# Kernel tuning notes

Hardware: AMD Instinct MI355X
Metric: run time of the kernel (lower is better)

## Reference

```python
import jax, jax.numpy as jnp
import numpy as np

# model dims (see init_kwargs)
HID = 2048
H = 16
Q_LORA = 768
KV_LORA = 512
QK_NOPE = 128
QK_ROPE = 64
QK_HEAD = QK_NOPE + QK_ROPE  # 192
V_DIM = 128
HI = 8        # indexer heads
DI = 128      # indexer head dim
TOPK = 512    # index_topk
EPS = 1e-5
B, S = 1, 2048


def rms_norm(x, w):
    return x * jax.lax.rsqrt(jnp.mean(x * x, -1, keepdims=True) + EPS) * w


def layer_norm(x, w, b):
    m = jnp.mean(x, -1, keepdims=True)
    v = jnp.mean((x - m) ** 2, -1, keepdims=True)
    return (x - m) * jax.lax.rsqrt(v + EPS) * w + b


def rotate_half(x):
    x1, x2 = jnp.split(x, 2, axis=-1)
    return jnp.concatenate([-x2, x1], axis=-1)


def rope_bshd(x, cos, sin):
    # x: [B,S,H,D], cos/sin: [B,S,D] -> broadcast over heads (unsqueeze_dim=2)
    return x * cos[:, :, None, :] + rotate_half(x) * sin[:, :, None, :]


def setup_inputs() -> dict:
    key = jax.random.key(0)
    ks = jax.random.split(key, 16)
    std = 0.02
    hidden_states = jax.random.normal(ks[0], (B, S, HID), jnp.float32)
    # real RoPE tables, theta=10000, head_dim=QK_ROPE
    inv_freq = 1.0 / (10000.0 ** (np.arange(0, QK_ROPE, 2, dtype=np.float32) / QK_ROPE))
    freqs = np.arange(S, dtype=np.float32)[:, None] * inv_freq[None, :]  # [S, ROPE/2]
    emb = np.concatenate([freqs, freqs], axis=-1)
    cos = jnp.asarray(np.cos(emb))[None]  # [1,S,ROPE]
    sin = jnp.asarray(np.sin(emb))[None]
    w = lambda k, shp: jax.random.normal(k, shp, jnp.float32) * std
    return {
        'hidden_states': hidden_states, 'cos': cos, 'sin': sin,
        'wq_a': w(ks[1], (Q_LORA, HID)),
        'q_a_norm_w': jnp.ones((Q_LORA,), jnp.float32),
        'wq_b': w(ks[2], (H * QK_HEAD, Q_LORA)),
        'wkv_a': w(ks[3], (KV_LORA + QK_ROPE, HID)),
        'kv_a_norm_w': jnp.ones((KV_LORA,), jnp.float32),
        'wkv_b': w(ks[4], (H * (QK_NOPE + V_DIM), KV_LORA)),
        'wo': w(ks[5], (HID, H * V_DIM)),
        'idx_wq_b': w(ks[6], (HI * DI, Q_LORA)),
        'idx_wk': w(ks[7], (DI, HID)),
        'idx_k_norm_w': jnp.ones((DI,), jnp.float32),
        'idx_k_norm_b': jnp.zeros((DI,), jnp.float32),
        'idx_weights_w': w(ks[8], (HI, HID)),
    }


def reference(hidden_states, cos, sin, wq_a, q_a_norm_w, wq_b, wkv_a, kv_a_norm_w,
              wkv_b, wo, idx_wq_b, idx_wk, idx_k_norm_w, idx_k_norm_b, idx_weights_w):
    b, s, _ = hidden_states.shape
    # ---- MLA projections ----
    q_lora = rms_norm(hidden_states @ wq_a.T, q_a_norm_w)              # [B,S,Q_LORA]
    q = (q_lora @ wq_b.T).reshape(b, s, H, QK_HEAD)
    q_nope, q_rope = jnp.split(q, [QK_NOPE], axis=-1)
    q_rope = rope_bshd(q_rope, cos, sin)

    kv = hidden_states @ wkv_a.T                                        # [B,S,KV_LORA+ROPE]
    kv_lat, k_rope = jnp.split(kv, [KV_LORA], axis=-1)
    k_rope = k_rope * cos + rotate_half(k_rope) * sin                   # shared MQA rope key [B,S,ROPE]
    kv_lat = rms_norm(kv_lat, kv_a_norm_w)
    kvb = (kv_lat @ wkv_b.T).reshape(b, s, H, QK_NOPE + V_DIM)
    k_nope, value = jnp.split(kvb, [QK_NOPE], axis=-1)

    queries = jnp.concatenate([q_nope, q_rope], axis=-1)                # [B,S,H,QK_HEAD]
    keys = jnp.concatenate(
        [k_nope, jnp.broadcast_to(k_rope[:, :, None, :], (b, s, H, QK_ROPE))], axis=-1)

    # ---- lightning indexer (DSA): per-query top-k KV selection ----
    iq = (q_lora @ idx_wq_b.T).reshape(b, s, HI, DI)
    iq_rot, iq_pass = jnp.split(iq, [QK_ROPE], axis=-1)
    iq = jnp.concatenate([rope_bshd(iq_rot, cos, sin), iq_pass], axis=-1)
    ik = layer_norm(hidden_states @ idx_wk.T, idx_k_norm_w, idx_k_norm_b)  # [B,S,DI]
    ik_rot, ik_pass = jnp.split(ik, [QK_ROPE], axis=-1)
    ik = jnp.concatenate([ik_rot * cos + rotate_half(ik_rot) * sin, ik_pass], axis=-1)

    iscores = jnp.einsum('bqhd,bkd->bqhk', iq, ik) * (DI ** -0.5)       # [B,S,HI,S]
    iw = (hidden_states @ idx_weights_w.T) * (HI ** -0.5)               # [B,S,HI]
    iscore = jnp.einsum('bqh,bqhk->bqk', iw, iscores)                   # [B,S,S]

    causal = jnp.tril(jnp.ones((s, s), bool))
    iscore = jnp.where(causal[None], iscore, -1e9)
    _, topk_idx = jax.lax.top_k(iscore, TOPK)                           # [B,S,TOPK]
    allow = jnp.zeros((b, s, s), bool).at[
        jnp.arange(b)[:, None, None], jnp.arange(s)[None, :, None], topk_idx].set(True)
    allow = allow & causal[None]                                        # topk AND causal

    # ---- masked attention ----
    scale = QK_HEAD ** -0.5
    scores = jnp.einsum('bqhd,bkhd->bhqk', queries, keys) * scale       # [B,H,S,S]
    scores = jnp.where(allow[:, None], scores, -jnp.inf)
    probs = jax.nn.softmax(scores, axis=-1)
    out = jnp.einsum('bhqk,bkhd->bqhd', probs, value).reshape(b, s, H * V_DIM)
    return out @ wo.T
```

## Files before the change

kernel.cpp:

```cpp
#include <hip/hip_runtime.h>
#include <hip/hip_bf16.h>
#include <stdint.h>
#include <math.h>

#define S_LEN 2048
#define HIDDEN 2048
#define NHEAD 16
#define QLORA 768
#define KVLORA 512
#define QKNOPE 128
#define QKROPE 64
#define QKHEAD 192
#define VDIM 128
#define HIN 8
#define DIN 128
#define TOPKN 512
#define EPSF 1e-5f
#define DLAT 576
#define SCALE_ATT 0.07216878364870322f

typedef __bf16 bf16x8 __attribute__((ext_vector_type(8)));
typedef float  f32x4  __attribute__((ext_vector_type(4)));

static __device__ __forceinline__ float wave_reduce_sum(float v) {
    #pragma unroll
    for (int off = 32; off > 0; off >>= 1) v += __shfl_down(v, off);
    return v;
}

static __device__ __forceinline__ void splitw(__bf16* __restrict__ H,
                                              __bf16* __restrict__ L,
                                              size_t idx, float v) {
    __bf16 h = (__bf16)v;
    H[idx] = h;
    L[idx] = (__bf16)(v - (float)h);
}

#define PREP_BLOCKS 17280
__global__ __launch_bounds__(256) void prep_all(
        const float* __restrict__ hid,     __bf16* hidH,  __bf16* hidL,
        const float* __restrict__ wq_a,    __bf16* wqaH,  __bf16* wqaL,
        const float* __restrict__ idx_wq_b,__bf16* iwqH,  __bf16* iwqL,
        const float* __restrict__ idx_wk,  __bf16* iwkH,  __bf16* iwkL,
        const float* __restrict__ wq_b,    __bf16* wq_b_bf,
        const float* __restrict__ wkv_a,   __bf16* wkv_a_bf,
        const float* __restrict__ wkv_b,   __bf16* wkv_b_bf,
        const float* __restrict__ wo,      __bf16* wo_bf,
        __bf16* wknt) {
    int b = blockIdx.x, tid = threadIdx.x;
    const float* src; __bf16 *dH = nullptr, *dL = nullptr, *dC = nullptr;
    int base;
    if (b < 4096)        { src = hid;      dH = hidH; dL = hidL; base = b; }
    else if (b < 5632)   { src = wq_a;     dH = wqaH; dL = wqaL; base = b - 4096; }
    else if (b < 6400)   { src = idx_wq_b; dH = iwqH; dL = iwqL; base = b - 5632; }
    else if (b < 6656)   { src = idx_wk;   dH = iwkH; dL = iwkL; base = b - 6400; }
    else if (b < 8960)   { src = wq_b;     dC = wq_b_bf;  base = b - 6656; }
    else if (b < 10112)  { src = wkv_a;    dC = wkv_a_bf; base = b - 8960; }
    else if (b < 12160)  { src = wkv_b;    dC = wkv_b_bf; base = b - 10112; }
    else if (b < 16256)  { src = wo;       dC = wo_bf;    base = b - 12160; }
    else {
        int e = ((b - 16256) * 256 + tid) * 4;
        int c = e & 511, d = (e >> 9) & 127, h = e >> 16;
        f32x4 v = *(const f32x4*)(wkv_b + ((size_t)(h * 256 + d)) * 512 + c);
        #pragma unroll
        for (int j = 0; j < 4; ++j)
            wknt[(size_t)h * 65536 + (c + j) * 128 + d] = (__bf16)v[j];
        return;
    }
    int i = (base * 256 + tid) * 4;
    f32x4 v = *(const f32x4*)(src + i);
    if (dC) {
        #pragma unroll
        for (int j = 0; j < 4; ++j) dC[i + j] = (__bf16)v[j];
    } else {
        #pragma unroll
        for (int j = 0; j < 4; ++j) splitw(dH, dL, i + j, v[j]);
    }
}

#define GBM 128
#define GBN 64
#define GBK 32
template <typename OutT>
__global__ __launch_bounds__(256) void gemm_s(const __bf16* __restrict__ A,
                                              const __bf16* __restrict__ B,
                                              OutT* __restrict__ C,
                                              int M, int N, int K,
                                              int lda, int ldb, int ldc,
                                              long sA, long sB, long sC) {
    A += (size_t)blockIdx.z * sA;
    B += (size_t)blockIdx.z * sB;
    C += (size_t)blockIdx.z * sC;
    __shared__ __bf16 sAs[GBM * GBK];
    __shared__ __bf16 sBs[GBN * GBK];
    int tid = threadIdx.x;
    int lane = tid & 63, wid = tid >> 6;
    int quad = lane >> 4, l16 = lane & 15;
    int wm = wid >> 1, wn = wid & 1;
    int row0 = blockIdx.y * GBM, col0 = blockIdx.x * GBN;

    f32x4 acc[4][2] = {};
    int am = tid >> 1, ah = tid & 1;
    int bn = tid >> 2, bq = tid & 3;

    for (int k0 = 0; k0 < K; k0 += GBK) {
        const uint4* ga = (const uint4*)(A + (size_t)(row0 + am) * lda + k0 + ah * 16);
        uint4* da = (uint4*)&sAs[am * GBK + ah * 16];
        da[0] = ga[0];
        da[1] = ga[1];
        *(uint4*)&sBs[bn * GBK + bq * 8] =
            *(const uint4*)(B + (size_t)(col0 + bn) * ldb + k0 + bq * 8);
        __syncthreads();
        bf16x8 af[4], bfr[2];
        #pragma unroll
        for (int mi = 0; mi < 4; ++mi)
            af[mi] = *(const bf16x8*)&sAs[(wm * 64 + mi * 16 + l16) * GBK + quad * 8];
        #pragma unroll
        for (int ni = 0; ni < 2; ++ni)
            bfr[ni] = *(const bf16x8*)&sBs[(wn * 32 + ni * 16 + l16) * GBK + quad * 8];
        #pragma unroll
        for (int mi = 0; mi < 4; ++mi)
            #pragma unroll
            for (int ni = 0; ni < 2; ++ni)
                acc[mi][ni] = __builtin_amdgcn_mfma_f32_16x16x32_bf16(
                    af[mi], bfr[ni], acc[mi][ni], 0, 0, 0);
        __syncthreads();
    }
    #pragma unroll
    for (int mi = 0; mi < 4; ++mi)
        #pragma unroll
        for (int ni = 0; ni < 2; ++ni)
            #pragma unroll
            for (int r = 0; r < 4; ++r) {
                int row = row0 + wm * 64 + mi * 16 + quad * 4 + r;
                int col = col0 + wn * 32 + ni * 16 + l16;
                C[(size_t)row * ldc + col] = (OutT)acc[mi][ni][r];
            }
}

template <bool CAUSAL>
__global__ __launch_bounds__(256) void gemm3(const __bf16* __restrict__ Ah,
                                             const __bf16* __restrict__ Al,
                                             const __bf16* __restrict__ Bh,
                                             const __bf16* __restrict__ Bl,
                                             float* __restrict__ C,
                                             int M, int N, int K,
                                             int lda, int ldb, int ldc,
                                             int row_base) {
    int row0 = blockIdx.y * GBM + row_base, col0 = blockIdx.x * GBN;
    if (CAUSAL && col0 > row0 + GBM - 1) return;
    __shared__ __bf16 sAh[GBM * GBK], sAl[GBM * GBK];
    __shared__ __bf16 sBh[GBN * GBK], sBl[GBN * GBK];
    int tid = threadIdx.x;
    int lane = tid & 63, wid = tid >> 6;
    int quad = lane >> 4, l16 = lane & 15;
    int wm = wid >> 1, wn = wid & 1;

    f32x4 acc[4][2] = {};
    int am = tid >> 1, ah = tid & 1;
    int bn = tid >> 2, bq = tid & 3;

    for (int k0 = 0; k0 < K; k0 += GBK) {
        size_t aoff = (size_t)(row0 + am) * lda + k0 + ah * 16;
        uint4* dah = (uint4*)&sAh[am * GBK + ah * 16];
        uint4* dal = (uint4*)&sAl[am * GBK + ah * 16];
        dah[0] = ((const uint4*)(Ah + aoff))[0];
        dah[1] = ((const uint4*)(Ah + aoff))[1];
        dal[0] = ((const uint4*)(Al + aoff))[0];
        dal[1] = ((const uint4*)(Al + aoff))[1];
        size_t boff = (size_t)(col0 + bn) * ldb + k0 + bq * 8;
        *(uint4*)&sBh[bn * GBK + bq * 8] = *(const uint4*)(Bh + boff);
        *(uint4*)&sBl[bn * GBK + bq * 8] = *(const uint4*)(Bl + boff);
        __syncthreads();
        bf16x8 afh[4], afl[4], bfh[2], bfl[2];
        #pragma unroll
        for (int mi = 0; mi < 4; ++mi) {
            int o = (wm * 64 + mi * 16 + l16) * GBK + quad * 8;
            afh[mi] = *(const bf16x8*)&sAh[o];
            afl[mi] = *(const bf16x8*)&sAl[o];
        }
        #pragma unroll
        for (int ni = 0; ni < 2; ++ni) {
            int o = (wn * 32 + ni * 16 + l16) * GBK + quad * 8;
            bfh[ni] = *(const bf16x8*)&sBh[o];
            bfl[ni] = *(const bf16x8*)&sBl[o];
        }
        #pragma unroll
        for (int mi = 0; mi < 4; ++mi)
            #pragma unroll
            for (int ni = 0; ni < 2; ++ni) {
                acc[mi][ni] = __builtin_amdgcn_mfma_f32_16x16x32_bf16(
                    afl[mi], bfh[ni], acc[mi][ni], 0, 0, 0);
                acc[mi][ni] = __builtin_amdgcn_mfma_f32_16x16x32_bf16(
                    afh[mi], bfl[ni], acc[mi][ni], 0, 0, 0);
                acc[mi][ni] = __builtin_amdgcn_mfma_f32_16x16x32_bf16(
                    afh[mi], bfh[ni], acc[mi][ni], 0, 0, 0);
            }
        __syncthreads();
    }
    #pragma unroll
    for (int mi = 0; mi < 4; ++mi)
        #pragma unroll
        for (int ni = 0; ni < 2; ++ni)
            #pragma unroll
            for (int r = 0; r < 4; ++r) {
                int row = row0 + wm * 64 + mi * 16 + quad * 4 + r;
                int col = col0 + wn * 32 + ni * 16 + l16;
                C[(size_t)row * ldc + col] = acc[mi][ni][r];
            }
}

__global__ __launch_bounds__(256) void rmsnorm_split(const float* __restrict__ x,
                                                     const float* __restrict__ w,
                                                     __bf16* __restrict__ yH,
                                                     __bf16* __restrict__ yL, int ncols) {
    int row = blockIdx.x, tid = threadIdx.x;
    const float* xr = x + (size_t)row * ncols;
    float ss = 0.f;
    for (int c = tid; c < ncols; c += 256) { float v = xr[c]; ss += v * v; }
    __shared__ float red[4];
    ss = wave_reduce_sum(ss);
    if ((tid & 63) == 0) red[tid >> 6] = ss;
    __syncthreads();
    float tot = red[0] + red[1] + red[2] + red[3];
    float inv = rsqrtf(tot / (float)ncols + EPSF);
    for (int c = tid; c < ncols; c += 256)
        splitw(yH, yL, (size_t)row * ncols + c, xr[c] * inv * w[c]);
}

__global__ __launch_bounds__(256) void rope_qeff(const __bf16* __restrict__ qbuf,
                                                 const float* __restrict__ cosT,
                                                 const float* __restrict__ sinT,
                                                 __bf16* __restrict__ qeff) {
    int s = blockIdx.x;
    for (int i = threadIdx.x; i < NHEAD * 32; i += 256) {
        int h = i >> 5, d = i & 31;
        const __bf16* base = qbuf + (size_t)s * (NHEAD * QKHEAD) + h * QKHEAD + QKNOPE;
        float x1 = (float)base[d], x2 = (float)base[d + 32];
        float c1 = cosT[s * 64 + d],      s1 = sinT[s * 64 + d];
        float c2 = cosT[s * 64 + d + 32], s2 = sinT[s * 64 + d + 32];
        __bf16* o = qeff + (size_t)s * (NHEAD * DLAT) + h * DLAT + 512;
        o[d]      = (__bf16)(x1 * c1 - x2 * s1);
        o[d + 32] = (__bf16)(x2 * c2 + x1 * s2);
    }
}

__global__ __launch_bounds__(256) void kv_post(const float* __restrict__ kv,
                                               const float* __restrict__ kvw,
                                               const float* __restrict__ cosT,
                                               const float* __restrict__ sinT,
                                               __bf16* __restrict__ klat) {
    int s = blockIdx.x, tid = threadIdx.x;
    const float* row = kv + (size_t)s * DLAT;
    float ss = 0.f;
    for (int c = tid; c < KVLORA; c += 256) { float v = row[c]; ss += v * v; }
    __shared__ float red[4];
    ss = wave_reduce_sum(ss);
    if ((tid & 63) == 0) red[tid >> 6] = ss;
    __syncthreads();
    float tot = red[0] + red[1] + red[2] + red[3];
    float inv = rsqrtf(tot / (float)KVLORA + EPSF);
    __bf16* orow = klat + (size_t)s * DLAT;
    for (int c = tid; c < KVLORA; c += 256)
        orow[c] = (__bf16)(row[c] * inv * kvw[c]);
    if (tid < 32) {
        int d = tid;
        float x1 = row[KVLORA + d], x2 = row[KVLORA + d + 32];
        float c1 = cosT[s * 64 + d],      s1 = sinT[s * 64 + d];
        float c2 = cosT[s * 64 + d + 32], s2 = sinT[s * 64 + d + 32];
        orow[512 + d]      = (__bf16)(x1 * c1 - x2 * s1);
        orow[512 + d + 32] = (__bf16)(x2 * c2 + x1 * s2);
    }
}

__global__ __launch_bounds__(128) void ik_post_split(const float* __restrict__ ikraw,
                                                     const float* __restrict__ w,
                                                     const float* __restrict__ b,
                                                     const float* __restrict__ cosT,
                                                     const float* __restrict__ sinT,
                                                     __bf16* __restrict__ ikH,
                                                     __bf16* __restrict__ ikL) {
    int s = blockIdx.x, tid = threadIdx.x;
    float x = ikraw[(size_t)s * DIN + tid];
    __shared__ float redA[2], redB[2], sy[DIN];
    float sm = wave_reduce_sum(x);
    if ((tid & 63) == 0) redA[tid >> 6] = sm;
    __syncthreads();
    float mean = (redA[0] + redA[1]) / (float)DIN;
    float dx = x - mean;
    float vs = wave_reduce_sum(dx * dx);
    if ((tid & 63) == 0) redB[tid >> 6] = vs;
    __syncthreads();
    float var = (redB[0] + redB[1]) / (float)DIN;
    sy[tid] = dx * rsqrtf(var + EPSF) * w[tid] + b[tid];
    __syncthreads();
    size_t ro = (size_t)s * DIN;
    if (tid < 32) {
        int d = tid;
        float c1 = cosT[s * 64 + d],      s1 = sinT[s * 64 + d];
        float c2 = cosT[s * 64 + d + 32], s2 = sinT[s * 64 + d + 32];
        splitw(ikH, ikL, ro + d,      sy[d] * c1 - sy[d + 32] * s1);
        splitw(ikH, ikL, ro + d + 32, sy[d + 32] * c2 + sy[d] * s2);
    } else if (tid >= 64) {
        splitw(ikH, ikL, ro + tid, sy[tid]);
    }
}

__global__ __launch_bounds__(128) void cq2(const float* __restrict__ iqraw,
                                           const float* __restrict__ hid,
                                           const float* __restrict__ iww,
                                           const float* __restrict__ cosT,
                                           const float* __restrict__ sinT,
                                           __bf16* __restrict__ cqH,
                                           __bf16* __restrict__ cqL) {
    int s = blockIdx.x, tid = threadIdx.x;
    int lane = tid & 63, wid = tid >> 6;
    __shared__ float red[2][HIN], siw[HIN];
    float a8[HIN] = {};
    const float* xr = hid + (size_t)s * HIDDEN;
    for (int c = tid; c < HIDDEN; c += 128) {
        float x = xr[c];
        #pragma unroll
        for (int h = 0; h < HIN; ++h) a8[h] += x * iww[h * HIDDEN + c];
    }
    #pragma unroll
    for (int h = 0; h < HIN; ++h) a8[h] = wave_reduce_sum(a8[h]);
    if (lane == 0)
        #pragma unroll
        for (int h = 0; h < HIN; ++h) red[wid][h] = a8[h];
    __syncthreads();
    if (tid < HIN) siw[tid] = red[0][tid] + red[1][tid];
    __syncthreads();
    int d = tid;
    float acc = 0.f;
    float c1 = 0.f, s1 = 0.f;
    if (d < 64) { c1 = cosT[s * 64 + d]; s1 = sinT[s * 64 + d]; }
    #pragma unroll
    for (int h = 0; h < HIN; ++h) {
        const float* base = iqraw + ((size_t)s * HIN + h) * DIN;
        float v;
        if (d < 32)       v = base[d] * c1 - base[d + 32] * s1;
        else if (d < 64)  v = base[d] * c1 + base[d - 32] * s1;
        else              v = base[d];
        acc += siw[h] * v;
    }
    splitw(cqH, cqL, (size_t)s * DIN + d, acc * 0.03125f);
}

__global__ __launch_bounds__(256) void topk_rows(const float* __restrict__ iscore,
                                                 int* __restrict__ topk) {
    int q = TOPKN + blockIdx.x;
    int n = q + 1;
    __shared__ uint32_t skey[S_LEN];
    __shared__ int hist[256];
    __shared__ int scan[256];
    __shared__ uint32_t sp;
    __shared__ int sr, pos;
    int tid = threadIdx.x;
    const float* row = iscore + (size_t)q * S_LEN;
    for (int i = tid; i < n; i += 256) {
        uint32_t u = __float_as_uint(row[i]);
        skey[i] = (u & 0x80000000u) ? ~u : (u | 0x80000000u);
    }
    __syncthreads();
    uint32_t prefix = 0;
    int remk = TOPKN;
    for (int pass = 0; pass < 4; ++pass) {
        int shift = 24 - 8 * pass;
        uint32_t pmask = pass ? (0xFFFFFFFFu << (shift + 8)) : 0u;
        hist[tid] = 0;
        __syncthreads();
        for (int i = tid; i < n; i += 256) {
            uint32_t u = skey[i];
            if ((u & pmask) == prefix) atomicAdd(&hist[(u >> shift) & 255], 1);
        }
        __syncthreads();
        scan[tid] = hist[tid];
        __syncthreads();
        for (int step = 1; step < 256; step <<= 1) {
            int v = (tid + step < 256) ? scan[tid + step] : 0;
            __syncthreads();
            scan[tid] += v;
            __syncthreads();
        }
        int Sb = scan[tid];
        int Snext = (tid < 255) ? scan[tid + 1] : 0;
        if (Sb >= remk && Snext < remk) {
            sp = prefix | ((uint32_t)tid << shift);
            sr = remk - Snext;
        }
        __syncthreads();
        prefix = sp; remk = sr;
        __syncthreads();
    }
    if (tid == 0) pos = 0;
    __syncthreads();
    int* orow = topk + (size_t)q * TOPKN;
    for (int i = tid; i < n; i += 256) {
        if (skey[i] > prefix) { int p = atomicAdd(&pos, 1); orow[p] = i; }
    }
    __syncthreads();
    int base = pos;
    int chunk = (n + 255) >> 8;
    int lo = tid * chunk, hiEnd = lo + chunk;
    if (hiEnd > n) hiEnd = n;
    int cnt = 0;
    for (int i = lo; i < hiEnd; ++i) cnt += (skey[i] == prefix);
    scan[tid] = cnt;
    __syncthreads();
    for (int step = 1; step < 256; step <<= 1) {
        int v = (tid >= step) ? scan[tid - step] : 0;
        __syncthreads();
        scan[tid] += v;
        __syncthreads();
    }
    int r = scan[tid] - cnt;
    for (int i = lo; i < hiEnd && r < remk; ++i) {
        if (skey[i] == prefix) { orow[base + r] = i; ++r; }
    }
}

#define SKS 584
__global__ __launch_bounds__(256) void attn2(const __bf16* __restrict__ qeff,
                                             const __bf16* __restrict__ klat,
                                             const int* __restrict__ topk,
                                             __bf16* __restrict__ o_lat) {
    int q = blockIdx.x;
    int tid = threadIdx.x;
    int lane = tid & 63, wid = tid >> 6;
    int l16 = lane & 15, quad = lane >> 4;
    int wn = wid & 1, wk = wid >> 1;

    __shared__ short sK[32 * SKS];
    __shared__ float s_part[2][16][37];
    __shared__ float s_S[16][37];
    __shared__ float s_m[16], s_l[16], s_alpha[16], s_inv[16];

    int L = (q < TOPKN) ? (q + 1) : TOPKN;
    int nt = (L + 31) >> 5;
    const int* idxr = topk + (size_t)q * TOPKN;

    bf16x8 qf[9];
    const __bf16* qrow = qeff + (size_t)q * (NHEAD * DLAT) + l16 * DLAT + wk * 288 + quad * 8;
    #pragma unroll
    for (int s = 0; s < 9; ++s) qf[s] = *(const bf16x8*)(qrow + s * 32);

    if (tid < 16) { s_m[tid] = -1e30f; s_l[tid] = 0.f; }

    f32x4 oacc[8];
    #pragma unroll
    for (int i = 0; i < 8; ++i) oacc[i] = (f32x4){0.f, 0.f, 0.f, 0.f};

    int srow = tid >> 3, schk = tid & 7;

    for (int t = 0; t < nt; ++t) {
        int ki = t * 32 + srow;
        int gk = 0;
        if (ki < L) gk = (q < TOPKN) ? ki : idxr[ki];
        const uint4* src = (const uint4*)(klat + (size_t)gk * DLAT) + schk * 9;
        uint4* dst = (uint4*)((char*)sK + srow * (SKS * 2) + schk * 144);
        #pragma unroll
        for (int c = 0; c < 9; ++c) dst[c] = src[c];
        __syncthreads();

        f32x4 sacc = {0.f, 0.f, 0.f, 0.f};
        const short* kbase = sK + (wn * 16 + l16) * SKS + wk * 288 + quad * 8;
        #pragma unroll
        for (int s = 0; s < 9; ++s) {
            bf16x8 kf = *(const bf16x8*)(kbase + s * 32);
            sacc = __builtin_amdgcn_mfma_f32_16x16x32_bf16(qf[s], kf, sacc, 0, 0, 0);
        }
        #pragma unroll
        for (int r = 0; r < 4; ++r)
            s_part[wk][quad * 4 + r][wn * 16 + l16] = sacc[r];
        __syncthreads();

        {
            int h = tid >> 4, k0 = (tid & 15) * 2;
            float v0 = -1e30f, v1 = -1e30f;
            if (t * 32 + k0 < L)
                v0 = (s_part[0][h][k0] + s_part[1][h][k0]) * SCALE_ATT;
            if (t * 32 + k0 + 1 < L)
                v1 = (s_part[0][h][k0 + 1] + s_part[1][h][k0 + 1]) * SCALE_ATT;
            float mt = fmaxf(v0, v1);
            #pragma unroll
            for (int o = 1; o < 16; o <<= 1) mt = fmaxf(mt, __shfl_xor(mt, o));
            float mold = s_m[h];
            float mnew = fmaxf(mold, mt);
            float p0 = __expf(v0 - mnew), p1 = __expf(v1 - mnew);
            float ls = p0 + p1;
            #pragma unroll
            for (int o = 1; o < 16; o <<= 1) ls += __shfl_xor(ls, o);
            s_S[h][k0] = p0; s_S[h][k0 + 1] = p1;
            if ((tid & 15) == 0) {
                float alpha = __expf(mold - mnew);
                s_alpha[h] = alpha;
                s_m[h] = mnew;
                s_l[h] = s_l[h] * alpha + ls;
            }
        }
        __syncthreads();

        f32x4 al4 = *(const f32x4*)&s_alpha[quad * 4];
        bf16x8 pf;
        #pragma unroll
        for (int j = 0; j < 8; ++j)
            pf[j] = (__bf16)s_S[l16][quad * 8 + (j ^ quad)];
        const __bf16* sKb = (const __bf16*)sK;
        #pragma unroll
        for (int n = 0; n < 8; ++n) {
            int dim = wid * 128 + n * 16 + l16;
            bf16x8 vf;
            #pragma unroll
            for (int j = 0; j < 8; ++j)
                vf[j] = sKb[(quad * 8 + (j ^ quad)) * SKS + dim];
            #pragma unroll
            for (int r = 0; r < 4; ++r) oacc[n][r] *= al4[r];
            oacc[n] = __builtin_amdgcn_mfma_f32_16x16x32_bf16(pf, vf, oacc[n], 0, 0, 0);
        }
        __syncthreads();
    }

    if (tid < 16) s_inv[tid] = 1.f / s_l[tid];
    __syncthreads();
    f32x4 inv4 = *(const f32x4*)&s_inv[quad * 4];
    #pragma unroll
    for (int n = 0; n < 8; ++n) {
        int dim = wid * 128 + n * 16 + l16;
        #pragma unroll
        for (int r = 0; r < 4; ++r) {
            int h = quad * 4 + r;
            o_lat[(size_t)q * 8192 + h * 512 + dim] = (__bf16)(oacc[n][r] * inv4[r]);
        }
    }
}

extern "C" void kernel_launch(void* const* d_in, const int* in_sizes, int n_in,
                              void* d_out, int out_size, void* d_ws, size_t ws_size,
                              hipStream_t stream) {
    const float* hid          = (const float*)d_in[0];
    const float* cosT         = (const float*)d_in[1];
    const float* sinT         = (const float*)d_in[2];
    const float* wq_a         = (const float*)d_in[3];
    const float* q_a_norm_w   = (const float*)d_in[4];
    const float* wq_b         = (const float*)d_in[5];
    const float* wkv_a        = (const float*)d_in[6];
    const float* kv_a_norm_w  = (const float*)d_in[7];
    const float* wkv_b        = (const float*)d_in[8];
    const float* wo           = (const float*)d_in[9];
    const float* idx_wq_b     = (const float*)d_in[10];
    const float* idx_wk       = (const float*)d_in[11];
    const float* idx_k_norm_w = (const float*)d_in[12];
    const float* idx_k_norm_b = (const float*)d_in[13];
    const float* idx_weights_w= (const float*)d_in[14];
    float* out = (float*)d_out;

    char* ws = (char*)d_ws;
    size_t off = 0;
    auto alloc = [&](size_t nbytes) {
        void* p = (void*)(ws + off);
        off += (nbytes + 255) & ~(size_t)255;
        return p;
    };
    float*  q_lora   = (float*) alloc((size_t)S_LEN * QLORA * 4);
    __bf16* qbuf_bf  = (__bf16*)alloc((size_t)S_LEN * NHEAD * QKHEAD * 2);
    float*  kv       = (float*) alloc((size_t)S_LEN * DLAT * 4);
    __bf16* klat_bf  = (__bf16*)alloc((size_t)S_LEN * DLAT * 2);
    __bf16* qeff_bf  = (__bf16*)alloc((size_t)S_LEN * NHEAD * DLAT * 2);
    int*    topk     = (int*)   alloc((size_t)S_LEN * TOPKN * 4);
    char* uB = (char*)alloc((size_t)S_LEN * HIDDEN * 2 + (size_t)DLAT * HIDDEN * 2);
    __bf16* hidH      = (__bf16*)uB;
    __bf16* wkv_a_bf  = (__bf16*)(uB + (size_t)S_LEN * HIDDEN * 2);
    __bf16* attn_o_bf = (__bf16*)uB;
    __bf16* hidL      = (__bf16*)alloc((size_t)S_LEN * HIDDEN * 2);
    char* uC = (char*)alloc((size_t)S_LEN * NHEAD * 512 * 2);
    __bf16* o_lat_bf = (__bf16*)uC;
    float* iqraw  = (float*)uC;
    float* ikraw  = (float*)(uC + 8388608);
    float* iscore = (float*)(uC + 11599872);
    __bf16* wq_b_bf  = (__bf16*)alloc((size_t)(NHEAD * QKHEAD) * QLORA * 2);
    __bf16* wkv_b_bf = (__bf16*)alloc((size_t)(NHEAD * 256) * KVLORA * 2);
    __bf16* wknt_bf  = (__bf16*)alloc((size_t)NHEAD * 512 * 128 * 2);
    __bf16* wo_bf    = (__bf16*)alloc((size_t)HIDDEN * (NHEAD * VDIM) * 2);
    __bf16* wqaH = (__bf16*)alloc((size_t)QLORA * HIDDEN * 2);
    __bf16* wqaL = (__bf16*)alloc((size_t)QLORA * HIDDEN * 2);
    __bf16* qlH  = (__bf16*)alloc((size_t)S_LEN * QLORA * 2);
    __bf16* qlL  = (__bf16*)alloc((size_t)S_LEN * QLORA * 2);
    __bf16* iwqH = (__bf16*)alloc((size_t)(HIN * DIN) * QLORA * 2);
    __bf16* iwqL = (__bf16*)alloc((size_t)(HIN * DIN) * QLORA * 2);
    __bf16* iwkH = (__bf16*)alloc((size_t)DIN * HIDDEN * 2);
    __bf16* iwkL = (__bf16*)alloc((size_t)DIN * HIDDEN * 2);
    __bf16* ikH  = (__bf16*)alloc((size_t)S_LEN * DIN * 2);
    __bf16* ikL  = (__bf16*)alloc((size_t)S_LEN * DIN * 2);
    __bf16* cqH  = (__bf16*)alloc((size_t)S_LEN * DIN * 2);
    __bf16* cqL  = (__bf16*)alloc((size_t)S_LEN * DIN * 2);
    (void)ws_size; (void)in_sizes; (void)n_in; (void)out_size;

    dim3 blk(256);

    prep_all<<<PREP_BLOCKS, blk, 0, stream>>>(
        hid, hidH, hidL, wq_a, wqaH, wqaL, idx_wq_b, iwqH, iwqL,
        idx_wk, iwkH, iwkL, wq_b, wq_b_bf, wkv_a, wkv_a_bf,
        wkv_b, wkv_b_bf, wo, wo_bf, wknt_bf);

    gemm3<false><<<dim3(QLORA / GBN, S_LEN / GBM), blk, 0, stream>>>(
        hidH, hidL, wqaH, wqaL, q_lora, S_LEN, QLORA, HIDDEN, HIDDEN, HIDDEN, QLORA, 0);
    rmsnorm_split<<<S_LEN, 256, 0, stream>>>(q_lora, q_a_norm_w, qlH, qlL, QLORA);
    gemm_s<__bf16><<<dim3((NHEAD * QKHEAD) / GBN, S_LEN / GBM, 1), blk, 0, stream>>>(
        qlH, wq_b_bf, qbuf_bf, S_LEN, NHEAD * QKHEAD, QLORA,
        QLORA, QLORA, NHEAD * QKHEAD, 0, 0, 0);
    rope_qeff<<<S_LEN, 256, 0, stream>>>(qbuf_bf, cosT, sinT, qeff_bf);
    gemm_s<__bf16><<<dim3(512 / GBN, S_LEN / GBM, NHEAD), blk, 0, stream>>>(
        qbuf_bf, wknt_bf, qeff_bf, S_LEN, 512, 128,
        NHEAD * QKHEAD, 128, NHEAD * DLAT, QKHEAD, 512 * 128, DLAT);
    gemm_s<float><<<dim3(DLAT / GBN, S_LEN / GBM, 1), blk, 0, stream>>>(
        hidH, wkv_a_bf, kv, S_LEN, DLAT, HIDDEN, HIDDEN, HIDDEN, DLAT, 0, 0, 0);
    kv_post<<<S_LEN, 256, 0, stream>>>(kv, kv_a_norm_w, cosT, sinT, klat_bf);
    gemm3<false><<<dim3((HIN * DIN) / GBN, S_LEN / GBM), blk, 0, stream>>>(
        qlH, qlL, iwqH, iwqL, iqraw, S_LEN, HIN * DIN, QLORA, QLORA, QLORA, HIN * DIN, 0);
    gemm3<false><<<dim3(DIN / GBN, S_LEN / GBM), blk, 0, stream>>>(
        hidH, hidL, iwkH, iwkL, ikraw, S_LEN, DIN, HIDDEN, HIDDEN, HIDDEN, DIN, 0);
    ik_post_split<<<S_LEN, 128, 0, stream>>>(ikraw, idx_k_norm_w, idx_k_norm_b,
                                             cosT, sinT, ikH, ikL);
    cq2<<<S_LEN, 128, 0, stream>>>(iqraw, hid, idx_weights_w, cosT, sinT, cqH, cqL);
    gemm3<true><<<dim3(S_LEN / GBN, (S_LEN - TOPKN) / GBM), blk, 0, stream>>>(
        cqH, cqL, ikH, ikL, iscore, S_LEN, S_LEN, DIN, DIN, DIN, S_LEN, TOPKN);
    topk_rows<<<S_LEN - TOPKN, 256, 0, stream>>>(iscore, topk);
    attn2<<<S_LEN, 256, 0, stream>>>(qeff_bf, klat_bf, topk, o_lat_bf);
    gemm_s<__bf16><<<dim3(VDIM / GBN, S_LEN / GBM, NHEAD), blk, 0, stream>>>(
        o_lat_bf, wkv_b_bf + 128 * 512, attn_o_bf, S_LEN, VDIM, 512,
        NHEAD * 512, 512, NHEAD * VDIM, 512, 256 * 512, VDIM);
    gemm_s<float><<<dim3(HIDDEN / GBN, S_LEN / GBM, 1), blk, 0, stream>>>(
        attn_o_bf, wo_bf, out, S_LEN, HIDDEN, NHEAD * VDIM,
        NHEAD * VDIM, NHEAD * VDIM, HIDDEN, 0, 0, 0);
}
```

Baseline: 669.5 us.

## Split-K q_a GEMM, fuse independent GEMMs and post-ops into combined launches

New measurement: 572.6 us. 14.5% less time.

```diff
diff --git a/kernel.cpp b/kernel.cpp
--- a/kernel.cpp
+++ b/kernel.cpp
@@ -82,22 +82,17 @@
 #define GBN 64
 #define GBK 32
 template <typename OutT>
-__global__ __launch_bounds__(256) void gemm_s(const __bf16* __restrict__ A,
-                                              const __bf16* __restrict__ B,
-                                              OutT* __restrict__ C,
-                                              int M, int N, int K,
-                                              int lda, int ldb, int ldc,
-                                              long sA, long sB, long sC) {
-    A += (size_t)blockIdx.z * sA;
-    B += (size_t)blockIdx.z * sB;
-    C += (size_t)blockIdx.z * sC;
+static __device__ __forceinline__ void gemm_s_core(
+        const __bf16* __restrict__ A, const __bf16* __restrict__ B,
+        OutT* __restrict__ C, int K, int lda, int ldb, int ldc,
+        int bx, int by) {
     __shared__ __bf16 sAs[GBM * GBK];
     __shared__ __bf16 sBs[GBN * GBK];
     int tid = threadIdx.x;
     int lane = tid & 63, wid = tid >> 6;
     int quad = lane >> 4, l16 = lane & 15;
     int wm = wid >> 1, wn = wid & 1;
-    int row0 = blockIdx.y * GBM, col0 = blockIdx.x * GBN;
+    int row0 = by * GBM, col0 = bx * GBN;
 
     f32x4 acc[4][2] = {};
     int am = tid >> 1, ah = tid & 1;
@@ -138,16 +133,24 @@
             }
 }
 
+template <typename OutT>
+__global__ __launch_bounds__(256) void gemm_s(const __bf16* __restrict__ A,
+                                              const __bf16* __restrict__ B,
+                                              OutT* __restrict__ C,
+                                              int K, int lda, int ldb, int ldc,
+                                              long sA, long sB, long sC) {
+    gemm_s_core<OutT>(A + (size_t)blockIdx.z * sA, B + (size_t)blockIdx.z * sB,
+                      C + (size_t)blockIdx.z * sC, K, lda, ldb, ldc,
+                      blockIdx.x, blockIdx.y);
+}
+
 template <bool CAUSAL>
-__global__ __launch_bounds__(256) void gemm3(const __bf16* __restrict__ Ah,
-                                             const __bf16* __restrict__ Al,
-                                             const __bf16* __restrict__ Bh,
-                                             const __bf16* __restrict__ Bl,
-                                             float* __restrict__ C,
-                                             int M, int N, int K,
-                                             int lda, int ldb, int ldc,
-                                             int row_base) {
-    int row0 = blockIdx.y * GBM + row_base, col0 = blockIdx.x * GBN;
+static __device__ __forceinline__ void gemm3_core(
+        const __bf16* __restrict__ Ah, const __bf16* __restrict__ Al,
+        const __bf16* __restrict__ Bh, const __bf16* __restrict__ Bl,
+        float* __restrict__ C, int K, int lda, int ldb, int ldc,
+        int row_base, int bx, int by) {
+    int row0 = by * GBM + row_base, col0 = bx * GBN;
     if (CAUSAL && col0 > row0 + GBM - 1) return;
     __shared__ __bf16 sAh[GBM * GBK], sAl[GBM * GBK];
     __shared__ __bf16 sBh[GBN * GBK], sBl[GBN * GBK];
@@ -210,30 +213,103 @@
             }
 }
 
-__global__ __launch_bounds__(256) void rmsnorm_split(const float* __restrict__ x,
-                                                     const float* __restrict__ w,
-                                                     __bf16* __restrict__ yH,
-                                                     __bf16* __restrict__ yL, int ncols) {
+__global__ __launch_bounds__(256) void gemm3_ks(const __bf16* __restrict__ Ah,
+                                                const __bf16* __restrict__ Al,
+                                                const __bf16* __restrict__ Bh,
+                                                const __bf16* __restrict__ Bl,
+                                                float* __restrict__ Cpart,
+                                                int Ksub, int lda, int ldb, int ldc,
+                                                long sC) {
+    int bz = blockIdx.z, koff = bz * Ksub;
+    gemm3_core<false>(Ah + koff, Al + koff, Bh + koff, Bl + koff,
+                      Cpart + (size_t)bz * sC, Ksub, lda, ldb, ldc, 0,
+                      blockIdx.x, blockIdx.y);
+}
+
+__global__ __launch_bounds__(256) void fused_mid(
+        const __bf16* __restrict__ qlH, const __bf16* __restrict__ qlL,
+        const __bf16* __restrict__ wq_b_bf, __bf16* __restrict__ qbuf_bf,
+        const __bf16* __restrict__ hidH, const __bf16* __restrict__ hidL,
+        const __bf16* __restrict__ wkv_a_bf, float* __restrict__ kv,
+        const __bf16* __restrict__ iwqH, const __bf16* __restrict__ iwqL,
+        float* __restrict__ iqraw,
+        const __bf16* __restrict__ iwkH, const __bf16* __restrict__ iwkL,
+        float* __restrict__ ikraw) {
+    int b = blockIdx.x;
+    if (b < 768) {
+        gemm_s_core<__bf16>(qlH, wq_b_bf, qbuf_bf, QLORA, QLORA, QLORA,
+                            NHEAD * QKHEAD, b % 48, b / 48);
+    } else if (b < 912) {
+        int r = b - 768;
+        gemm_s_core<float>(hidH, wkv_a_bf, kv, HIDDEN, HIDDEN, HIDDEN, DLAT,
+                           r % 9, r / 9);
+    } else if (b < 1168) {
+        int r = b - 912;
+        gemm3_core<false>(qlH, qlL, iwqH, iwqL, iqraw, QLORA, QLORA, QLORA,
+                          HIN * DIN, 0, r & 15, r >> 4);
+    } else {
+        int r = b - 1168;
+        gemm3_core<false>(hidH, hidL, iwkH, iwkL, ikraw, HIDDEN, HIDDEN, HIDDEN,
+                          DIN, 0, r & 1, r >> 1);
+    }
+}
+
+__global__ __launch_bounds__(256) void fused2(
+        const __bf16* __restrict__ qbuf_bf, const __bf16* __restrict__ wknt,
+        __bf16* __restrict__ qeff,
+        const __bf16* __restrict__ cqH, const __bf16* __restrict__ cqL,
+        const __bf16* __restrict__ ikH, const __bf16* __restrict__ ikL,
+        float* __restrict__ iscore) {
+    int b = blockIdx.x;
+    if (b < 2048) {
+        int bx = b & 7, by = (b >> 3) & 15, bz = b >> 7;
+        gemm_s_core<__bf16>(qbuf_bf + bz * QKHEAD, wknt + (size_t)bz * 512 * 128,
+                            qeff + bz * DLAT, 128, NHEAD * QKHEAD, 128,
+                            NHEAD * DLAT, bx, by);
+    } else {
+        int r = b - 2048;
+        gemm3_core<true>(cqH, cqL, ikH, ikL, iscore, DIN, DIN, DIN, S_LEN,
+                         TOPKN, r & 31, r >> 5);
+    }
+}
+
+__global__ __launch_bounds__(256) void rmsnorm_split4(const float* __restrict__ p,
+                                                      long ps,
+                                                      const float* __restrict__ w,
+                                                      __bf16* __restrict__ yH,
+                                                      __bf16* __restrict__ yL, int ncols) {
     int row = blockIdx.x, tid = threadIdx.x;
-    const float* xr = x + (size_t)row * ncols;
+    const float* p0 = p + (size_t)row * ncols;
     float ss = 0.f;
-    for (int c = tid; c < ncols; c += 256) { float v = xr[c]; ss += v * v; }
+    for (int c = tid; c < ncols; c += 256) {
+        float v = p0[c] + p0[ps + c] + p0[2 * ps + c] + p0[3 * ps + c];
+        ss += v * v;
+    }
     __shared__ float red[4];
     ss = wave_reduce_sum(ss);
     if ((tid & 63) == 0) red[tid >> 6] = ss;
     __syncthreads();
     float tot = red[0] + red[1] + red[2] + red[3];
     float inv = rsqrtf(tot / (float)ncols + EPSF);
-    for (int c = tid; c < ncols; c += 256)
-        splitw(yH, yL, (size_t)row * ncols + c, xr[c] * inv * w[c]);
-}
-
-__global__ __launch_bounds__(256) void rope_qeff(const __bf16* __restrict__ qbuf,
-                                                 const float* __restrict__ cosT,
-                                                 const float* __restrict__ sinT,
-                                                 __bf16* __restrict__ qeff) {
-    int s = blockIdx.x;
-    for (int i = threadIdx.x; i < NHEAD * 32; i += 256) {
+    for (int c = tid; c < ncols; c += 256) {
+        float v = p0[c] + p0[ps + c] + p0[2 * ps + c] + p0[3 * ps + c];
+        splitw(yH, yL, (size_t)row * ncols + c, v * inv * w[c]);
+    }
+}
+
+__global__ __launch_bounds__(256) void fused_post(
+        const __bf16* __restrict__ qbuf, __bf16* __restrict__ qeff,
+        const float* __restrict__ kv, const float* __restrict__ kvw,
+        __bf16* __restrict__ klat,
+        const float* __restrict__ ikraw, const float* __restrict__ lnw,
+        const float* __restrict__ lnb, __bf16* __restrict__ ikH, __bf16* __restrict__ ikL,
+        const float* __restrict__ iqraw, const float* __restrict__ hid,
+        const float* __restrict__ iww, __bf16* __restrict__ cqH, __bf16* __restrict__ cqL,
+        const float* __restrict__ cosT, const float* __restrict__ sinT) {
+    int s = blockIdx.x, tid = threadIdx.x;
+    int lane = tid & 63, wid = tid >> 6;
+
+    for (int i = tid; i < NHEAD * 32; i += 256) {
         int h = i >> 5, d = i & 31;
         const __bf16* base = qbuf + (size_t)s * (NHEAD * QKHEAD) + h * QKHEAD + QKNOPE;
         float x1 = (float)base[d], x2 = (float)base[d + 32];
@@ -243,108 +319,92 @@
         o[d]      = (__bf16)(x1 * c1 - x2 * s1);
         o[d + 32] = (__bf16)(x2 * c2 + x1 * s2);
     }
-}
-
-__global__ __launch_bounds__(256) void kv_post(const float* __restrict__ kv,
-                                               const float* __restrict__ kvw,
-                                               const float* __restrict__ cosT,
-                                               const float* __restrict__ sinT,
-                                               __bf16* __restrict__ klat) {
-    int s = blockIdx.x, tid = threadIdx.x;
-    const float* row = kv + (size_t)s * DLAT;
-    float ss = 0.f;
-    for (int c = tid; c < KVLORA; c += 256) { float v = row[c]; ss += v * v; }
-    __shared__ float red[4];
-    ss = wave_reduce_sum(ss);
-    if ((tid & 63) == 0) red[tid >> 6] = ss;
-    __syncthreads();
-    float tot = red[0] + red[1] + red[2] + red[3];
-    float inv = rsqrtf(tot / (float)KVLORA + EPSF);
-    __bf16* orow = klat + (size_t)s * DLAT;
-    for (int c = tid; c < KVLORA; c += 256)
-        orow[c] = (__bf16)(row[c] * inv * kvw[c]);
-    if (tid < 32) {
-        int d = tid;
-        float x1 = row[KVLORA + d], x2 = row[KVLORA + d + 32];
-        float c1 = cosT[s * 64 + d],      s1 = sinT[s * 64 + d];
-        float c2 = cosT[s * 64 + d + 32], s2 = sinT[s * 64 + d + 32];
-        orow[512 + d]      = (__bf16)(x1 * c1 - x2 * s1);
-        orow[512 + d + 32] = (__bf16)(x2 * c2 + x1 * s2);
-    }
-}
-
-__global__ __launch_bounds__(128) void ik_post_split(const float* __restrict__ ikraw,
-                                                     const float* __restrict__ w,
-                                                     const float* __restrict__ b,
-                                                     const float* __restrict__ cosT,
-                                                     const float* __restrict__ sinT,
-                                                     __bf16* __restrict__ ikH,
-                                                     __bf16* __restrict__ ikL) {
-    int s = blockIdx.x, tid = threadIdx.x;
-    float x = ikraw[(size_t)s * DIN + tid];
-    __shared__ float redA[2], redB[2], sy[DIN];
-    float sm = wave_reduce_sum(x);
-    if ((tid & 63) == 0) redA[tid >> 6] = sm;
-    __syncthreads();
-    float mean = (redA[0] + redA[1]) / (float)DIN;
-    float dx = x - mean;
-    float vs = wave_reduce_sum(dx * dx);
-    if ((tid & 63) == 0) redB[tid >> 6] = vs;
-    __syncthreads();
-    float var = (redB[0] + redB[1]) / (float)DIN;
-    sy[tid] = dx * rsqrtf(var + EPSF) * w[tid] + b[tid];
-    __syncthreads();
-    size_t ro = (size_t)s * DIN;
-    if (tid < 32) {
-        int d = tid;
-        float c1 = cosT[s * 64 + d],      s1 = sinT[s * 64 + d];
-        float c2 = cosT[s * 64 + d + 32], s2 = sinT[s * 64 + d + 32];
-        splitw(ikH, ikL, ro + d,      sy[d] * c1 - sy[d + 32] * s1);
-        splitw(ikH, ikL, ro + d + 32, sy[d + 32] * c2 + sy[d] * s2);
-    } else if (tid >= 64) {
-        splitw(ikH, ikL, ro + tid, sy[tid]);
-    }
-}
-
-__global__ __launch_bounds__(128) void cq2(const float* __restrict__ iqraw,
-                                           const float* __restrict__ hid,
-                                           const float* __restrict__ iww,
-                                           const float* __restrict__ cosT,
-                                           const float* __restrict__ sinT,
-                                           __bf16* __restrict__ cqH,
-                                           __bf16* __restrict__ cqL) {
-    int s = blockIdx.x, tid = threadIdx.x;
-    int lane = tid & 63, wid = tid >> 6;
-    __shared__ float red[2][HIN], siw[HIN];
-    float a8[HIN] = {};
-    const float* xr = hid + (size_t)s * HIDDEN;
-    for (int c = tid; c < HIDDEN; c += 128) {
-        float x = xr[c];
-        #pragma unroll
-        for (int h = 0; h < HIN; ++h) a8[h] += x * iww[h * HIDDEN + c];
-    }
-    #pragma unroll
-    for (int h = 0; h < HIN; ++h) a8[h] = wave_reduce_sum(a8[h]);
-    if (lane == 0)
-        #pragma unroll
-        for (int h = 0; h < HIN; ++h) red[wid][h] = a8[h];
-    __syncthreads();
-    if (tid < HIN) siw[tid] = red[0][tid] + red[1][tid];
-    __syncthreads();
-    int d = tid;
-    float acc = 0.f;
-    float c1 = 0.f, s1 = 0.f;
-    if (d < 64) { c1 = cosT[s * 64 + d]; s1 = sinT[s * 64 + d]; }
-    #pragma unroll
-    for (int h = 0; h < HIN; ++h) {
-        const float* base = iqraw + ((size_t)s * HIN + h) * DIN;
-        float v;
-        if (d < 32)       v = base[d] * c1 - base[d + 32] * s1;
-        else if (d < 64)  v = base[d] * c1 + base[d - 32] * s1;
-        else              v = base[d];
-        acc += siw[h] * v;
-    }
-    splitw(cqH, cqL, (size_t)s * DIN + d, acc * 0.03125f);
+
+    {
+        const float* row = kv + (size_t)s * DLAT;
+        float ss = 0.f;
+        for (int c = tid; c < KVLORA; c += 256) { float v = row[c]; ss += v * v; }
+        __shared__ float redB[4];
+        ss = wave_reduce_sum(ss);
+        if (lane == 0) redB[wid] = ss;
+        __syncthreads();
+        float tot = redB[0] + redB[1] + redB[2] + redB[3];
+        float inv = rsqrtf(tot / (float)KVLORA + EPSF);
+        __bf16* orow = klat + (size_t)s * DLAT;
+        for (int c = tid; c < KVLORA; c += 256)
+            orow[c] = (__bf16)(row[c] * inv * kvw[c]);
+        if (tid < 32) {
+            int d = tid;
+            float x1 = row[KVLORA + d], x2 = row[KVLORA + d + 32];
+            float c1 = cosT[s * 64 + d],      s1 = sinT[s * 64 + d];
+            float c2 = cosT[s * 64 + d + 32], s2 = sinT[s * 64 + d + 32];
+            orow[512 + d]      = (__bf16)(x1 * c1 - x2 * s1);
+            orow[512 + d + 32] = (__bf16)(x2 * c2 + x1 * s2);
+        }
+    }
+
+    {
+        float x = (tid < DIN) ? ikraw[(size_t)s * DIN + tid] : 0.f;
+        __shared__ float redC1[4], redC2[4], sy[DIN];
+        float sm = wave_reduce_sum(x);
+        if (lane == 0) redC1[wid] = sm;
+        __syncthreads();
+        float mean = (redC1[0] + redC1[1] + redC1[2] + redC1[3]) / (float)DIN;
+        float dx = (tid < DIN) ? (x - mean) : 0.f;
+        float vs = wave_reduce_sum(dx * dx);
+        if (lane == 0) redC2[wid] = vs;
+        __syncthreads();
+        float var = (redC2[0] + redC2[1] + redC2[2] + redC2[3]) / (float)DIN;
+        if (tid < DIN) sy[tid] = dx * rsqrtf(var + EPSF) * lnw[tid] + lnb[tid];
+        __syncthreads();
+        size_t ro = (size_t)s * DIN;
+        if (tid < 32) {
+            int d = tid;
+            float c1 = cosT[s * 64 + d],      s1 = sinT[s * 64 + d];
+            float c2 = cosT[s * 64 + d + 32], s2 = sinT[s * 64 + d + 32];
+            splitw(ikH, ikL, ro + d,      sy[d] * c1 - sy[d + 32] * s1);
+            splitw(ikH, ikL, ro + d + 32, sy[d + 32] * c2 + sy[d] * s2);
+        } else if (tid >= 64 && tid < DIN) {
+            splitw(ikH, ikL, ro + tid, sy[tid]);
+        }
+        __syncthreads();
+    }
+
+    {
+        __shared__ float redD[4][HIN], siw[HIN];
+        float a8[HIN] = {};
+        const float* xr = hid + (size_t)s * HIDDEN;
+        for (int c = tid; c < HIDDEN; c += 256) {
+            float x = xr[c];
+            #pragma unroll
+            for (int h = 0; h < HIN; ++h) a8[h] += x * iww[h * HIDDEN + c];
+        }
+        #pragma unroll
+        for (int h = 0; h < HIN; ++h) a8[h] = wave_reduce_sum(a8[h]);
+        if (lane == 0)
+            #pragma unroll
+            for (int h = 0; h < HIN; ++h) redD[wid][h] = a8[h];
+        __syncthreads();
+        if (tid < HIN)
+            siw[tid] = redD[0][tid] + redD[1][tid] + redD[2][tid] + redD[3][tid];
+        __syncthreads();
+        if (tid < DIN) {
+            int d = tid;
+            float acc = 0.f;
+            float c1 = 0.f, s1 = 0.f;
+            if (d < 64) { c1 = cosT[s * 64 + d]; s1 = sinT[s * 64 + d]; }
+            #pragma unroll
+            for (int h = 0; h < HIN; ++h) {
+                const float* base = iqraw + ((size_t)s * HIN + h) * DIN;
+                float v;
+                if (d < 32)       v = base[d] * c1 - base[d + 32] * s1;
+                else if (d < 64)  v = base[d] * c1 + base[d - 32] * s1;
+                else              v = base[d];
+                acc += siw[h] * v;
+            }
+            splitw(cqH, cqL, (size_t)s * DIN + d, acc * 0.03125f);
+        }
+    }
 }
 
 __global__ __launch_bounds__(256) void topk_rows(const float* __restrict__ iscore,
@@ -425,7 +485,7 @@
                                              const __bf16* __restrict__ klat,
                                              const int* __restrict__ topk,
                                              __bf16* __restrict__ o_lat) {
-    int q = blockIdx.x;
+    int q = (blockIdx.x * 997) & (S_LEN - 1);
     int tid = threadIdx.x;
     int lane = tid & 63, wid = tid >> 6;
     int l16 = lane & 15, quad = lane >> 4;
@@ -433,7 +493,7 @@
 
     __shared__ short sK[32 * SKS];
     __shared__ float s_part[2][16][37];
-    __shared__ float s_S[16][37];
+    __shared__ float s_S[16][38];
     __shared__ float s_m[16], s_l[16], s_alpha[16], s_inv[16];
 
     int L = (q < TOPKN) ? (q + 1) : TOPKN;
@@ -491,7 +551,7 @@
             float ls = p0 + p1;
             #pragma unroll
             for (int o = 1; o < 16; o <<= 1) ls += __shfl_xor(ls, o);
-            s_S[h][k0] = p0; s_S[h][k0 + 1] = p1;
+            *(float2*)&s_S[h][k0] = make_float2(p0, p1);
             if ((tid & 15) == 0) {
                 float alpha = __expf(mold - mnew);
                 s_alpha[h] = alpha;
@@ -503,9 +563,14 @@
 
         f32x4 al4 = *(const f32x4*)&s_alpha[quad * 4];
         bf16x8 pf;
-        #pragma unroll
-        for (int j = 0; j < 8; ++j)
-            pf[j] = (__bf16)s_S[l16][quad * 8 + (j ^ quad)];
+        int qhi = quad & 2, qlo = quad & 1;
+        #pragma unroll
+        for (int p = 0; p < 4; ++p) {
+            float2 v = *(const float2*)&s_S[l16][quad * 8 + ((2 * p) ^ qhi)];
+            float e0 = qlo ? v.y : v.x, e1 = qlo ? v.x : v.y;
+            pf[2 * p]     = (__bf16)e0;
+            pf[2 * p + 1] = (__bf16)e1;
+        }
         const __bf16* sKb = (const __bf16*)sK;
         #pragma unroll
         for (int n = 0; n < 8; ++n) {
@@ -562,7 +627,6 @@
         off += (nbytes + 255) & ~(size_t)255;
         return p;
     };
-    float*  q_lora   = (float*) alloc((size_t)S_LEN * QLORA * 4);
     __bf16* qbuf_bf  = (__bf16*)alloc((size_t)S_LEN * NHEAD * QKHEAD * 2);
     float*  kv       = (float*) alloc((size_t)S_LEN * DLAT * 4);
     __bf16* klat_bf  = (__bf16*)alloc((size_t)S_LEN * DLAT * 2);
@@ -574,6 +638,7 @@
     __bf16* attn_o_bf = (__bf16*)uB;
     __bf16* hidL      = (__bf16*)alloc((size_t)S_LEN * HIDDEN * 2);
     char* uC = (char*)alloc((size_t)S_LEN * NHEAD * 512 * 2);
+    float*  qpart    = (float*)uC;
     __bf16* o_lat_bf = (__bf16*)uC;
     float* iqraw  = (float*)uC;
     float* ikraw  = (float*)(uC + 8388608);
@@ -603,34 +668,32 @@
         idx_wk, iwkH, iwkL, wq_b, wq_b_bf, wkv_a, wkv_a_bf,
         wkv_b, wkv_b_bf, wo, wo_bf, wknt_bf);
 
-    gemm3<false><<<dim3(QLORA / GBN, S_LEN / GBM), blk, 0, stream>>>(
-        hidH, hidL, wqaH, wqaL, q_lora, S_LEN, QLORA, HIDDEN, HIDDEN, HIDDEN, QLORA, 0);
-    rmsnorm_split<<<S_LEN, 256, 0, stream>>>(q_lora, q_a_norm_w, qlH, qlL, QLORA);
-    gemm_s<__bf16><<<dim3((NHEAD * QKHEAD) / GBN, S_LEN / GBM, 1), blk, 0, stream>>>(
-        qlH, wq_b_bf, qbuf_bf, S_LEN, NHEAD * QKHEAD, QLORA,
-        QLORA, QLORA, NHEAD * QKHEAD, 0, 0, 0);
-    rope_qeff<<<S_LEN, 256, 0, stream>>>(qbuf_bf, cosT, sinT, qeff_bf);
-    gemm_s<__bf16><<<dim3(512 / GBN, S_LEN / GBM, NHEAD), blk, 0, stream>>>(
-        qbuf_bf, wknt_bf, qeff_bf, S_LEN, 512, 128,
-        NHEAD * QKHEAD, 128, NHEAD * DLAT, QKHEAD, 512 * 128, DLAT);
-    gemm_s<float><<<dim3(DLAT / GBN, S_LEN / GBM, 1), blk, 0, stream>>>(
-        hidH, wkv_a_bf, kv, S_LEN, DLAT, HIDDEN, HIDDEN, HIDDEN, DLAT, 0, 0, 0);
-    kv_post<<<S_LEN, 256, 0, stream>>>(kv, kv_a_norm_w, cosT, sinT, klat_bf);
-    gemm3<false><<<dim3((HIN * DIN) / GBN, S_LEN / GBM), blk, 0, stream>>>(
-        qlH, qlL, iwqH, iwqL, iqraw, S_LEN, HIN * DIN, QLORA, QLORA, QLORA, HIN * DIN, 0);
-    gemm3<false><<<dim3(DIN / GBN, S_LEN / GBM), blk, 0, stream>>>(
-        hidH, hidL, iwkH, iwkL, ikraw, S_LEN, DIN, HIDDEN, HIDDEN, HIDDEN, DIN, 0);
-    ik_post_split<<<S_LEN, 128, 0, stream>>>(ikraw, idx_k_norm_w, idx_k_norm_b,
-                                             cosT, sinT, ikH, ikL);
-    cq2<<<S_LEN, 128, 0, stream>>>(iqraw, hid, idx_weights_w, cosT, sinT, cqH, cqL);
-    gemm3<true><<<dim3(S_LEN / GBN, (S_LEN - TOPKN) / GBM), blk, 0, stream>>>(
-        cqH, cqL, ikH, ikL, iscore, S_LEN, S_LEN, DIN, DIN, DIN, S_LEN, TOPKN);
+    gemm3_ks<<<dim3(QLORA / GBN, S_LEN / GBM, 4), blk, 0, stream>>>(
+        hidH, hidL, wqaH, wqaL, qpart, HIDDEN / 4, HIDDEN, HIDDEN, QLORA,
+        (long)S_LEN * QLORA);
+    rmsnorm_split4<<<S_LEN, 256, 0, stream>>>(qpart, (long)S_LEN * QLORA,
+                                              q_a_norm_w, qlH, qlL, QLORA);
+
+    fused_mid<<<1200, blk, 0, stream>>>(qlH, qlL, wq_b_bf, qbuf_bf,
+                                        hidH, hidL, wkv_a_bf, kv,
+                                        iwqH, iwqL, iqraw, iwkH, iwkL, ikraw);
+
+    fused_post<<<S_LEN, 256, 0, stream>>>(qbuf_bf, qeff_bf, kv, kv_a_norm_w, klat_bf,
+                                          ikraw, idx_k_norm_w, idx_k_norm_b, ikH, ikL,
+                                          iqraw, hid, idx_weights_w, cqH, cqL,
+                                          cosT, sinT);
+
+    fused2<<<2048 + 384, blk, 0, stream>>>(qbuf_bf, wknt_bf, qeff_bf,
+                                           cqH, cqL, ikH, ikL, iscore);
+
     topk_rows<<<S_LEN - TOPKN, 256, 0, stream>>>(iscore, topk);
+
     attn2<<<S_LEN, 256, 0, stream>>>(qeff_bf, klat_bf, topk, o_lat_bf);
+
     gemm_s<__bf16><<<dim3(VDIM / GBN, S_LEN / GBM, NHEAD), blk, 0, stream>>>(
-        o_lat_bf, wkv_b_bf + 128 * 512, attn_o_bf, S_LEN, VDIM, 512,
+        o_lat_bf, wkv_b_bf + 128 * 512, attn_o_bf, 512,
         NHEAD * 512, 512, NHEAD * VDIM, 512, 256 * 512, VDIM);
     gemm_s<float><<<dim3(HIDDEN / GBN, S_LEN / GBM, 1), blk, 0, stream>>>(
-        attn_o_bf, wo_bf, out, S_LEN, HIDDEN, NHEAD * VDIM,
+        attn_o_bf, wo_bf, out, NHEAD * VDIM,
         NHEAD * VDIM, NHEAD * VDIM, HIDDEN, 0, 0, 0);
 }
```
